# Optimization experiments

Hardware: AMD Instinct MI355X
Metric: run time of the kernel (lower is better)

Reference implementation:

```python
import jax, jax.numpy as jnp
import numpy as np
from math import ceil

N = 20000   # nodes
E = 320000  # edges
D = 128     # num_features == num_hidden
K = ceil(N * 0.1)  # 2000 PMA seeds


def _gcn(x, W, b, src, dst):
    # PyG GCNConv: add self-loops, symmetric deg^-1/2 normalization, sum-aggregate, bias
    n = x.shape[0]
    sl = jnp.arange(n)
    s = jnp.concatenate([src, sl])
    d = jnp.concatenate([dst, sl])
    deg = jax.ops.segment_sum(jnp.ones((s.shape[0],), x.dtype), d, num_segments=n)
    dinv = jax.lax.rsqrt(jnp.maximum(deg, 1e-12))
    norm = dinv[s] * dinv[d]
    h = x @ W
    return jax.ops.segment_sum(h[s] * norm[:, None], d, num_segments=n) + b


def _ln(x, g, b):
    m = jnp.mean(x, -1, keepdims=True)
    v = jnp.var(x, -1, keepdims=True)
    return (x - m) * jax.lax.rsqrt(v + 1e-5) * g + b


def setup_inputs() -> dict:
    key = jax.random.key(0)
    ks = jax.random.split(key, 32)
    w = lambda i, shape: jax.random.normal(ks[i], shape, jnp.float32) * 0.05
    z = lambda shape: jnp.zeros(shape, jnp.float32)
    o = lambda shape: jnp.ones(shape, jnp.float32)
    return {
        "x": jax.random.normal(ks[0], (N, D), jnp.float32),
        "edge_index": jax.random.randint(ks[1], (2, E), 0, N),
        "batch": jnp.zeros((N,), jnp.int32),
        "W1": w(2, (D, D)), "b1": z((D,)),
        "W2": w(3, (D, D)), "b2": z((D,)),
        "S": w(4, (1, K, D)),
        "Wq": w(5, (D, D)), "bq": z((D,)),
        "Wk": w(6, (D, D)), "bk": z((D,)),
        "Wv": w(7, (D, D)), "bv": z((D,)),
        "Wo": w(8, (D, D)), "bo": z((D,)),
        "g0": o((D,)), "be0": z((D,)),
        "g1": o((D,)), "be1": z((D,)),
        "Wl": w(9, (D, D)), "bl": z((D,)),
        "W3": w(10, (D, D)), "b3": z((D,)),
        "W4": w(11, (D, D)), "b4": z((D,)),
        "W5": w(12, (D, D)), "b5": z((D,)),
    }


def reference(x, edge_index, batch, W1, b1, W2, b2, S, Wq, bq, Wk, bk, Wv, bv,
              Wo, bo, g0, be0, g1, be1, Wl, bl, W3, b3, W4, b4, W5, b5):
    src, dst = edge_index[0], edge_index[1]
    h = jax.nn.relu(_gcn(x, W1, b1, src, dst))
    h = jax.nn.relu(_gcn(h, W2, b2, src, dst))
    # B=1 dense batch: mask all-true -> additive attention mask is 0
    Q = S @ Wq + bq                        # [1,K,D]
    Kd = _gcn(h, Wk, bk, src, dst)[None]   # [1,N,D]  (mab_conv='GCN')
    Vd = _gcn(h, Wv, bv, src, dst)[None]   # [1,N,D]
    score = jnp.einsum('bkd,bnd->bkn', Q, Kd) / jnp.sqrt(jnp.float32(D))
    A = jax.nn.softmax(score, axis=1)      # cluster=True: softmax over seed dim
    out = Q + jnp.einsum('bkn,bnd->bkd', A, Vd)
    out = _ln(out, g0, be0)
    out = out + jax.nn.relu(out @ Wo + bo)
    out = _ln(out, g1, be1)
    xl = out @ Wl + bl                     # [1,K,D]
    x_out = jnp.einsum('bkn,bkd->bnd', A, xl)[0]  # attn^T @ x -> [N,D], mask all-true
    h = jax.nn.relu(_gcn(x_out, W3, b3, src, dst))
    h = jax.nn.relu(_gcn(h, W4, b4, src, dst))
    return _gcn(h, W5, b5, src, dst)       # [N,D]
```

## Files before the change

kernel.cpp:

```cpp
#include <hip/hip_runtime.h>

#define NN 20000
#define EE 320000
#define KK 2000
#define KP 2048
#define SCALE 0.08838834764831845f
#define ZSPLIT 16
#define ACHUNKS 625

typedef const float* cfp;
typedef __attribute__((ext_vector_type(8))) short sh8;
typedef __attribute__((ext_vector_type(4))) float f32x4;

static __device__ __forceinline__ float4 ld4(const float* p){ return *reinterpret_cast<const float4*>(p); }
static __device__ __forceinline__ void st4(float* p, float4 v){ *reinterpret_cast<float4*>(p) = v; }

static __device__ __forceinline__ unsigned short f2bf(float f){
    unsigned int u = __float_as_uint(f);
    u = (u + 0x7FFFu + ((u >> 16) & 1u)) >> 16;
    return (unsigned short)u;
}
static __device__ __forceinline__ float bf2f(unsigned short h){
    return __uint_as_float(((unsigned int)h) << 16);
}
static __device__ __forceinline__ sh8 lds8(const unsigned short* p){ return *reinterpret_cast<const sh8*>(p); }

__global__ __launch_bounds__(256) void k_count(const int* dst, int* deg){
    int i = blockIdx.x*256 + threadIdx.x;
    if (i < EE) atomicAdd(&deg[dst[i]], 1);
}

__global__ __launch_bounds__(256) void k_dinv(const int* deg, float* dinv){
    int n = blockIdx.x*256 + threadIdx.x;
    if (n < NN) dinv[n] = rsqrtf((float)deg[n] + 1.0f);
}

__global__ __launch_bounds__(1024) void k_scan(const int* cnt, int* rows){
    __shared__ int part[1024];
    int t = threadIdx.x;
    int base = t*20;
    int s = 0;
    for (int i = 0; i < 20; ++i){ int idx = base+i; if (idx < NN) s += cnt[idx]; }
    part[t] = s; __syncthreads();
    for (int off = 1; off < 1024; off <<= 1){
        int v = (t >= off) ? part[t-off] : 0;
        __syncthreads();
        part[t] += v;
        __syncthreads();
    }
    int run = part[t] - s;
    for (int i = 0; i < 20; ++i){
        int idx = base+i;
        if (idx < NN){ rows[idx] = run; run += cnt[idx]; }
    }
    if (t == 0) rows[NN] = EE;
}

__global__ __launch_bounds__(256) void k_fill(const int* src, const int* dst, const int* rows,
                                              int* cursor, int* col){
    int i = blockIdx.x*256 + threadIdx.x;
    if (i < EE){
        int d = dst[i];
        int pos = rows[d] + atomicAdd(&cursor[d], 1);
        col[pos] = src[i];
    }
}

__global__ __launch_bounds__(256) void conv_wT(cfp w0, cfp w1, cfp w2, cfp w3, cfp w4, cfp w5, cfp w6,
                                               unsigned short* wts){
    const float* in;
    switch (blockIdx.z){
        case 0: in = w0; break; case 1: in = w1; break; case 2: in = w2; break;
        case 3: in = w3; break; case 4: in = w4; break; case 5: in = w5; break;
        default: in = w6; break;
    }
    unsigned short* out = wts + (size_t)blockIdx.z*16384;
    __shared__ float t[64][65];
    int r0 = blockIdx.x*64, c0 = blockIdx.y*64;
    int tid = threadIdx.x;
    for (int i = tid; i < 64*16; i += 256){
        int r = i >> 4, c4 = (i & 15) * 4;
        float4 v = ld4(in + (size_t)(r0+r)*128 + c0 + c4);
        t[r][c4+0]=v.x; t[r][c4+1]=v.y; t[r][c4+2]=v.z; t[r][c4+3]=v.w;
    }
    __syncthreads();
    for (int i = tid; i < 64*16; i += 256){
        int c = i >> 4, r4 = (i & 15) * 4;
        ushort4 o;
        o.x = f2bf(t[r4+0][c]); o.y = f2bf(t[r4+1][c]);
        o.z = f2bf(t[r4+2][c]); o.w = f2bf(t[r4+3][c]);
        *reinterpret_cast<ushort4*>(out + (size_t)(c0+c)*128 + r0 + r4) = o;
    }
}

__global__ __launch_bounds__(512) void gemm128(const float* __restrict__ A, const float* __restrict__ Wm,
                                               float* __restrict__ C, int M,
                                               const float* bias, const float* resid, int relu){
    __shared__ __align__(16) float Ws[128*132];
    __shared__ float As[64*129];
    int tid = threadIdx.x;
    int r0 = blockIdx.x*64;
    for (int i = tid; i < 128*32; i += 512){
        int r = i >> 5, c4 = (i & 31) * 4;
        float4 v = ld4(Wm + r*128 + c4);
        st4(&Ws[r*132 + c4], v);
    }
    for (int i = tid; i < 64*32; i += 512){
        int r = i >> 5, c4 = (i & 31) * 4;
        float4 v = (r0 + r < M) ? ld4(A + (size_t)(r0+r)*128 + c4) : make_float4(0,0,0,0);
        As[r*129 + c4+0] = v.x; As[r*129 + c4+1] = v.y;
        As[r*129 + c4+2] = v.z; As[r*129 + c4+3] = v.w;
    }
    __syncthreads();
    int a = tid >> 5;
    int b = tid & 31;
    float acc[4][4] = {};
    #pragma unroll 4
    for (int d = 0; d < 128; ++d){
        float4 w = ld4(&Ws[d*132 + 4*b]);
        float wv[4] = {w.x, w.y, w.z, w.w};
        float av[4];
        #pragma unroll
        for (int i = 0; i < 4; ++i) av[i] = As[(4*a+i)*129 + d];
        #pragma unroll
        for (int i = 0; i < 4; ++i)
            #pragma unroll
            for (int j = 0; j < 4; ++j)
                acc[i][j] += av[i]*wv[j];
    }
    int cc = 4*b;
    #pragma unroll
    for (int i = 0; i < 4; ++i){
        int r = r0 + 4*a + i;
        if (r < M){
            float v[4];
            #pragma unroll
            for (int j = 0; j < 4; ++j) v[j] = acc[i][j];
            if (bias){
                #pragma unroll
                for (int j = 0; j < 4; ++j) v[j] += bias[cc+j];
            }
            if (relu){
                #pragma unroll
                for (int j = 0; j < 4; ++j) v[j] = fmaxf(v[j], 0.f);
            }
            if (resid){
                float4 rv = ld4(resid + (size_t)r*128 + cc);
                v[0]+=rv.x; v[1]+=rv.y; v[2]+=rv.z; v[3]+=rv.w;
            }
            st4(C + (size_t)r*128 + cc, make_float4(v[0],v[1],v[2],v[3]));
        }
    }
}

__global__ __launch_bounds__(256) void tgemm(const unsigned short* __restrict__ A, int M,
                                             const unsigned short* __restrict__ Wt,
                                             const float* __restrict__ rscale,
                                             unsigned short* __restrict__ C){
    int tid = threadIdx.x;
    int wave = tid >> 6, lane = tid & 63;
    int wm = wave >> 1, wn = wave & 1;
    int m_base = blockIdx.x*64 + wm*32;
    int n_base = blockIdx.y*64 + wn*32;
    int l15 = lane & 15;
    int roff = (lane >> 4) * 8;
    const unsigned short* ap0 = A + (size_t)(m_base + l15)*128 + roff;
    const unsigned short* ap1 = ap0 + 16*128;
    const unsigned short* b0p = Wt + (size_t)(n_base + l15)*128 + roff;
    const unsigned short* b1p = b0p + 16*128;
    f32x4 acc00 = (f32x4)0.f, acc01 = (f32x4)0.f, acc10 = (f32x4)0.f, acc11 = (f32x4)0.f;
    #pragma unroll
    for (int r = 0; r < 128; r += 32){
        sh8 a0 = lds8(ap0 + r);
        sh8 a1 = lds8(ap1 + r);
        sh8 b0 = lds8(b0p + r);
        sh8 b1 = lds8(b1p + r);
        acc00 = __builtin_amdgcn_mfma_f32_16x16x32_bf16(a0, b0, acc00, 0, 0, 0);
        acc01 = __builtin_amdgcn_mfma_f32_16x16x32_bf16(a0, b1, acc01, 0, 0, 0);
        acc10 = __builtin_amdgcn_mfma_f32_16x16x32_bf16(a1, b0, acc10, 0, 0, 0);
        acc11 = __builtin_amdgcn_mfma_f32_16x16x32_bf16(a1, b1, acc11, 0, 0, 0);
    }
    int rq = (lane >> 4) * 4;
    f32x4 accs[2][2] = {{acc00, acc01},{acc10, acc11}};
    #pragma unroll
    for (int mi = 0; mi < 2; ++mi){
        #pragma unroll
        for (int ni = 0; ni < 2; ++ni){
            f32x4 a = accs[mi][ni];
            int gn = n_base + ni*16 + l15;
            #pragma unroll
            for (int reg = 0; reg < 4; ++reg){
                int gm = m_base + mi*16 + rq + reg;
                if (gm < M) C[(size_t)gm*128 + gn] = f2bf(a[reg] * (rscale ? rscale[gm] : 1.f));
            }
        }
    }
}

__global__ __launch_bounds__(256) void gcn_agg_bf(const unsigned short* __restrict__ y, const float* __restrict__ dinv,
                                                  const int* __restrict__ rows, const int* __restrict__ col,
                                                  const float* __restrict__ bias, void* __restrict__ outv,
                                                  int relu, int out_fp32){
    int wid = (int)((blockIdx.x*256 + threadIdx.x) >> 6);
    int lane = threadIdx.x & 63;
    if (wid >= NN) return;
    int f = lane*2;
    ushort2 u = *reinterpret_cast<const ushort2*>(y + (size_t)wid*128 + f);
    float ax = bf2f(u.x), ay = bf2f(u.y);
    int s = rows[wid], e = rows[wid+1];
    int j = s;
    int e8 = s + ((e - s) & ~7);
    for (; j < e8; j += 8){
        ushort2 v[8];
        #pragma unroll
        for (int q = 0; q < 8; ++q){
            int c = col[j+q];
            v[q] = *reinterpret_cast<const ushort2*>(y + (size_t)c*128 + f);
        }
        #pragma unroll
        for (int q = 0; q < 8; ++q){ ax += bf2f(v[q].x); ay += bf2f(v[q].y); }
    }
    for (; j < e; ++j){
        int c0 = col[j];
        ushort2 v0 = *reinterpret_cast<const ushort2*>(y + (size_t)c0*128 + f);
        ax += bf2f(v0.x); ay += bf2f(v0.y);
    }
    float dn = dinv[wid];
    float ox = ax*dn + bias[f];
    float oy = ay*dn + bias[f+1];
    if (relu){ ox = fmaxf(ox, 0.f); oy = fmaxf(oy, 0.f); }
    if (out_fp32){
        *reinterpret_cast<float2*>((float*)outv + (size_t)wid*128 + f) = make_float2(ox, oy);
    } else {
        ushort2 o; o.x = f2bf(ox); o.y = f2bf(oy);
        *reinterpret_cast<ushort2*>((unsigned short*)outv + (size_t)wid*128 + f) = o;
    }
}

__global__ __launch_bounds__(256) void conv_bf16(const float* __restrict__ in, unsigned short* __restrict__ out, int n4){
    int i = blockIdx.x*256 + threadIdx.x;
    if (i < n4){
        float4 v = ld4(in + (size_t)i*4);
        ushort4 o;
        o.x = f2bf(v.x); o.y = f2bf(v.y); o.z = f2bf(v.z); o.w = f2bf(v.w);
        *reinterpret_cast<ushort4*>(out + (size_t)i*4) = o;
    }
}

__global__ __launch_bounds__(256) void conv_bf16_T(const float* __restrict__ in, unsigned short* __restrict__ out,
                                                   int M, int ldout, const float* __restrict__ rscale){
    __shared__ float t[64][65];
    int r0 = blockIdx.x*64, c0 = blockIdx.y*64;
    int tid = threadIdx.x;
    for (int i = tid; i < 64*16; i += 256){
        int r = i >> 4, c4 = (i & 15) * 4;
        float4 v = (r0 + r < M) ? ld4(in + (size_t)(r0+r)*128 + c0 + c4) : make_float4(0,0,0,0);
        if (rscale && r0 + r < M){
            float sc = rscale[r0 + r];
            v.x *= sc; v.y *= sc; v.z *= sc; v.w *= sc;
        }
        t[r][c4+0]=v.x; t[r][c4+1]=v.y; t[r][c4+2]=v.z; t[r][c4+3]=v.w;
    }
    __syncthreads();
    for (int i = tid; i < 64*16; i += 256){
        int c = i >> 4, r4 = (i & 15) * 4;
        if (r0 + r4 < M){
            ushort4 o;
            o.x = f2bf(t[r4+0][c]); o.y = f2bf(t[r4+1][c]);
            o.z = f2bf(t[r4+2][c]); o.w = f2bf(t[r4+3][c]);
            *reinterpret_cast<ushort4*>(out + (size_t)(c0+c)*ldout + r0 + r4) = o;
        }
    }
}

__global__ __launch_bounds__(256) void k_rcp32(const float* __restrict__ zp, const float* __restrict__ dinv,
                                               float* __restrict__ zinv, float* __restrict__ zdinv){
    int n = blockIdx.x*256 + threadIdx.x;
    if (n < NN){
        float s = 0.f;
        #pragma unroll
        for (int y = 0; y < 32; ++y) s += zp[(size_t)y*NN + n];
        float zi = 1.f / s;
        zinv[n] = zi;
        zdinv[n] = zi * dinv[n];
    }
}

__global__ __launch_bounds__(256) void s_gemm_exp(const unsigned short* __restrict__ Kb,
                                                  const unsigned short* __restrict__ Qb2,
                                                  unsigned short* __restrict__ E, float* __restrict__ zpart){
    __shared__ unsigned short Es[64*68];
    int tid = threadIdx.x;
    int wave = tid >> 6, lane = tid & 63;
    int wm = wave >> 1, wn = wave & 1;
    int n_blk = blockIdx.x*64, k_blk = blockIdx.y*64;
    int l15 = lane & 15;
    int roff = (lane >> 4) * 8;
    const unsigned short* ap0 = Kb + (size_t)(n_blk + wm*32 + l15)*128 + roff;
    const unsigned short* ap1 = ap0 + 16*128;
    const unsigned short* bp0 = Qb2 + (size_t)(k_blk + wn*32 + l15)*128 + roff;
    const unsigned short* bp1 = bp0 + 16*128;
    f32x4 acc00 = (f32x4)0.f, acc01 = (f32x4)0.f, acc10 = (f32x4)0.f, acc11 = (f32x4)0.f;
    #pragma unroll
    for (int r = 0; r < 128; r += 32){
        sh8 a0 = lds8(ap0 + r);
        sh8 a1 = lds8(ap1 + r);
        sh8 b0 = lds8(bp0 + r);
        sh8 b1 = lds8(bp1 + r);
        acc00 = __builtin_amdgcn_mfma_f32_16x16x32_bf16(a0, b0, acc00, 0, 0, 0);
        acc01 = __builtin_amdgcn_mfma_f32_16x16x32_bf16(a0, b1, acc01, 0, 0, 0);
        acc10 = __builtin_amdgcn_mfma_f32_16x16x32_bf16(a1, b0, acc10, 0, 0, 0);
        acc11 = __builtin_amdgcn_mfma_f32_16x16x32_bf16(a1, b1, acc11, 0, 0, 0);
    }
    int rq = (lane >> 4) * 4;
    f32x4 accs[2][2] = {{acc00, acc01},{acc10, acc11}};
    #pragma unroll
    for (int mi = 0; mi < 2; ++mi){
        #pragma unroll
        for (int ni = 0; ni < 2; ++ni){
            f32x4 a = accs[mi][ni];
            int c_loc = wn*32 + ni*16 + l15;
            bool kv = (k_blk + c_loc) < KK;
            #pragma unroll
            for (int reg = 0; reg < 4; ++reg){
                int r_loc = wm*32 + mi*16 + rq + reg;
                float e = kv ? __expf(a[reg]*SCALE) : 0.f;
                Es[r_loc*68 + c_loc] = f2bf(e);
            }
        }
    }
    __syncthreads();
    if (tid < 64){
        int n = n_blk + tid;
        if (n < NN){
            float s = 0.f;
            #pragma unroll 8
            for (int j = 0; j < 64; ++j) s += bf2f(Es[tid*68 + j]);
            zpart[(size_t)blockIdx.y*NN + n] = s;
        }
    }
    for (int i = tid; i < 512; i += 256){
        int r = i >> 3, c8 = (i & 7) * 8;
        if (n_blk + r < NN){
            ushort4 lo = *reinterpret_cast<const ushort4*>(&Es[r*68 + c8]);
            ushort4 hi = *reinterpret_cast<const ushort4*>(&Es[r*68 + c8 + 4]);
            unsigned short* dst = E + (size_t)(n_blk + r)*KP + k_blk + c8;
            *reinterpret_cast<ushort4*>(dst) = lo;
            *reinterpret_cast<ushort4*>(dst + 4) = hi;
        }
    }
}

__global__ __launch_bounds__(256) void attn_gemm(const unsigned short* __restrict__ E,
                                                 const unsigned short* __restrict__ Vt,
                                                 float* __restrict__ part){
    __shared__ unsigned short As[64*36];
    int tid = threadIdx.x;
    int wave = tid >> 6, lane = tid & 63;
    int kk0 = blockIdx.x*64;
    int per = (ACHUNKS + ZSPLIT - 1) / ZSPLIT;
    int c0 = blockIdx.y*per;
    int c1 = min(ACHUNKS, c0 + per);
    int l15 = lane & 15;
    int q8 = (lane >> 4) * 8;
    int d0 = wave*32;
    int n_l = tid & 31;
    int k8 = (tid >> 5) * 8;
    f32x4 acc[4][2];
    #pragma unroll
    for (int g = 0; g < 4; ++g){ acc[g][0] = (f32x4)0.f; acc[g][1] = (f32x4)0.f; }
    const unsigned short* ebase = E + (size_t)n_l*KP + kk0 + k8;
    const unsigned short* vb0p = Vt + (size_t)(d0 + l15)*NN + q8;
    const unsigned short* vb1p = vb0p + (size_t)16*NN;
    sh8 etmp = lds8(ebase + (size_t)c0*32*KP);
    sh8 vb0 = lds8(vb0p + c0*32);
    sh8 vb1 = lds8(vb1p + c0*32);
    for (int ch = c0; ch < c1; ++ch){
        unsigned short tmp[8];
        *reinterpret_cast<sh8*>(tmp) = etmp;
        #pragma unroll
        for (int j = 0; j < 8; ++j) As[(k8 + j)*36 + n_l] = tmp[j];
        __syncthreads();
        sh8 etn = (sh8)0, vbn0 = (sh8)0, vbn1 = (sh8)0;
        if (ch + 1 < c1){
            etn  = lds8(ebase + (size_t)(ch+1)*32*KP);
            vbn0 = lds8(vb0p + (ch+1)*32);
            vbn1 = lds8(vb1p + (ch+1)*32);
        }
        #pragma unroll
        for (int g = 0; g < 4; ++g){
            const unsigned short* ap = &As[(g*16 + l15)*36 + q8];
            union { struct { ushort4 lo, hi; } u; sh8 v; } af;
            af.u.lo = *reinterpret_cast<const ushort4*>(ap);
            af.u.hi = *reinterpret_cast<const ushort4*>(ap + 4);
            acc[g][0] = __builtin_amdgcn_mfma_f32_16x16x32_bf16(af.v, vb0, acc[g][0], 0, 0, 0);
            acc[g][1] = __builtin_amdgcn_mfma_f32_16x16x32_bf16(af.v, vb1, acc[g][1], 0, 0, 0);
        }
        __syncthreads();
        etmp = etn; vb0 = vbn0; vb1 = vbn1;
    }
    float* pbase = part + (size_t)blockIdx.y*KK*128;
    int rq = (lane >> 4) * 4;
    #pragma unroll
    for (int g = 0; g < 4; ++g){
        #pragma unroll
        for (int ni = 0; ni < 2; ++ni){
            int d = d0 + ni*16 + l15;
            #pragma unroll
            for (int reg = 0; reg < 4; ++reg){
                int kk = kk0 + g*16 + rq + reg;
                if (kk < KK) pbase[(size_t)kk*128 + d] = acc[g][ni][reg];
            }
        }
    }
}

__global__ __launch_bounds__(256) void xout_gemm(const unsigned short* __restrict__ E,
                                                 const unsigned short* __restrict__ B,
                                                 float* __restrict__ xpart){
    int tid = threadIdx.x;
    int wave = tid >> 6, lane = tid & 63;
    int wm = wave >> 1, wn = wave & 1;
    int m_base = blockIdx.x*64 + wm*32;
    int n_base = blockIdx.y*64 + wn*32;
    int kz = blockIdx.z*1024;
    int l15 = lane & 15;
    int roff = (lane >> 4) * 8;
    const unsigned short* ap0 = E + (size_t)(m_base + l15)*KP + kz + roff;
    const unsigned short* ap1 = ap0 + (size_t)16*KP;
    const unsigned short* bp0 = B + (size_t)(n_base + l15)*KP + kz + roff;
    const unsigned short* bp1 = bp0 + (size_t)16*KP;
    f32x4 acc00 = (f32x4)0.f, acc01 = (f32x4)0.f, acc10 = (f32x4)0.f, acc11 = (f32x4)0.f;
    sh8 a0 = lds8(ap0),      a1 = lds8(ap1),      a2 = lds8(ap0 + 32), a3 = lds8(ap1 + 32);
    sh8 b0 = lds8(bp0),      b1 = lds8(bp1),      b2 = lds8(bp0 + 32), b3 = lds8(bp1 + 32);
    for (int r = 0; r < 1024; r += 64){
        int rn = r + 64;
        sh8 na0 = (sh8)0, na1 = (sh8)0, na2 = (sh8)0, na3 = (sh8)0;
        sh8 nb0 = (sh8)0, nb1 = (sh8)0, nb2 = (sh8)0, nb3 = (sh8)0;
        if (rn < 1024){
            na0 = lds8(ap0 + rn);      na1 = lds8(ap1 + rn);
            na2 = lds8(ap0 + rn + 32); na3 = lds8(ap1 + rn + 32);
            nb0 = lds8(bp0 + rn);      nb1 = lds8(bp1 + rn);
            nb2 = lds8(bp0 + rn + 32); nb3 = lds8(bp1 + rn + 32);
        }
        acc00 = __builtin_amdgcn_mfma_f32_16x16x32_bf16(a0, b0, acc00, 0, 0, 0);
        acc01 = __builtin_amdgcn_mfma_f32_16x16x32_bf16(a0, b1, acc01, 0, 0, 0);
        acc10 = __builtin_amdgcn_mfma_f32_16x16x32_bf16(a1, b0, acc10, 0, 0, 0);
        acc11 = __builtin_amdgcn_mfma_f32_16x16x32_bf16(a1, b1, acc11, 0, 0, 0);
        acc00 = __builtin_amdgcn_mfma_f32_16x16x32_bf16(a2, b2, acc00, 0, 0, 0);
        acc01 = __builtin_amdgcn_mfma_f32_16x16x32_bf16(a2, b3, acc01, 0, 0, 0);
        acc10 = __builtin_amdgcn_mfma_f32_16x16x32_bf16(a3, b2, acc10, 0, 0, 0);
        acc11 = __builtin_amdgcn_mfma_f32_16x16x32_bf16(a3, b3, acc11, 0, 0, 0);
        a0 = na0; a1 = na1; a2 = na2; a3 = na3;
        b0 = nb0; b1 = nb1; b2 = nb2; b3 = nb3;
    }
    float* pbase = xpart + (size_t)blockIdx.z*NN*128;
    int rq = (lane >> 4) * 4;
    f32x4 accs[2][2] = {{acc00, acc01},{acc10, acc11}};
    #pragma unroll
    for (int mi = 0; mi < 2; ++mi){
        #pragma unroll
        for (int ni = 0; ni < 2; ++ni){
            f32x4 a = accs[mi][ni];
            int gn = n_base + ni*16 + l15;
            #pragma unroll
            for (int reg = 0; reg < 4; ++reg){
                int gm = m_base + mi*16 + rq + reg;
                if (gm < NN) pbase[(size_t)gm*128 + gn] = a[reg];
            }
        }
    }
}

__global__ __launch_bounds__(256) void xred(const float* __restrict__ xp, const float* __restrict__ zdinv,
                                            unsigned short* __restrict__ out){
    int i = blockIdx.x*256 + threadIdx.x;
    if (i < NN*32){
        int row = i >> 5;
        float4 p0 = ld4(xp + (size_t)i*4);
        float4 p1 = ld4(xp + (size_t)NN*128 + (size_t)i*4);
        float sc = zdinv[row];
        ushort4 o;
        o.x = f2bf((p0.x + p1.x)*sc);
        o.y = f2bf((p0.y + p1.y)*sc);
        o.z = f2bf((p0.z + p1.z)*sc);
        o.w = f2bf((p0.w + p1.w)*sc);
        *reinterpret_cast<ushort4*>(out + (size_t)i*4) = o;
    }
}

__global__ __launch_bounds__(128) void ln_ker(const float* __restrict__ in, int nparts,
                                              const float* __restrict__ resid,
                                              const float* __restrict__ g, const float* __restrict__ be,
                                              float* __restrict__ out){
    __shared__ float rs[128], rq[128];
    int r = blockIdx.x, t = threadIdx.x;
    float v = 0.f;
    for (int p = 0; p < nparts; ++p) v += in[(size_t)p*KK*128 + r*128 + t];
    if (resid) v += resid[r*128 + t];
    rs[t] = v; rq[t] = v*v;
    __syncthreads();
    for (int off = 64; off > 0; off >>= 1){
        if (t < off){ rs[t] += rs[t+off]; rq[t] += rq[t+off]; }
        __syncthreads();
    }
    float mean = rs[0]*(1.f/128.f);
    float var = rq[0]*(1.f/128.f) - mean*mean;
    out[r*128 + t] = (v - mean)*rsqrtf(var + 1e-5f)*g[t] + be[t];
}

extern "C" void kernel_launch(void* const* d_in, const int* in_sizes, int n_in,
                              void* d_out, int out_size, void* d_ws, size_t ws_size,
                              hipStream_t stream){
    cfp x  = (cfp)d_in[0];
    const int* ei = (const int*)d_in[1];
    const int* esrc = ei;
    const int* edst = ei + EE;
    cfp W1=(cfp)d_in[3], b1=(cfp)d_in[4], W2=(cfp)d_in[5], b2=(cfp)d_in[6];
    cfp S =(cfp)d_in[7];
    cfp Wq=(cfp)d_in[8],  bq=(cfp)d_in[9],  Wk=(cfp)d_in[10], bk=(cfp)d_in[11];
    cfp Wv=(cfp)d_in[12], bv=(cfp)d_in[13], Wo=(cfp)d_in[14], bo=(cfp)d_in[15];
    cfp g0=(cfp)d_in[16], be0=(cfp)d_in[17], g1=(cfp)d_in[18], be1=(cfp)d_in[19];
    cfp Wl=(cfp)d_in[20], bl=(cfp)d_in[21], W3=(cfp)d_in[22], b3=(cfp)d_in[23];
    cfp W4=(cfp)d_in[24], b4=(cfp)d_in[25], W5=(cfp)d_in[26], b5=(cfp)d_in[27];

    char* wsb = (char*)d_ws;
    const size_t MB = 1048576;
    int*   deg    = (int*)  (wsb + 0);
    float* dinv   = (float*)(wsb + 81920);
    int*   rows   = (int*)  (wsb + 163840);
    int*   cursor = (int*)  (wsb + 245760);
    int*   col    = (int*)  (wsb + 327680);
    float* Qb     = (float*)(wsb + 2*MB);
    float* o1     = (float*)(wsb + 3*MB);
    float* o2     = (float*)(wsb + 4*MB);
    float* o3     = (float*)(wsb + 5*MB);
    float* xlb    = (float*)(wsb + 6*MB);
    float* zpart  = (float*)(wsb + 7*MB);
    float* zinv   = (float*)(wsb + 10*MB);
    float* zdinv  = (float*)(wsb + 10*MB + 131072);
    unsigned short* Wts  = (unsigned short*)(wsb + 10*MB + 262144);
    unsigned short* Qbf  = (unsigned short*)(wsb + 11*MB);
    unsigned short* xlt3 = (unsigned short*)(wsb + 11*MB + 524288);
    unsigned short* xbf = (unsigned short*)(wsb + 12*MB);
    unsigned short* h1  = (unsigned short*)(wsb + 17*MB);
    unsigned short* h2  = (unsigned short*)(wsb + 22*MB);
    unsigned short* ybuf= (unsigned short*)(wsb + 27*MB);
    unsigned short* Kbf = (unsigned short*)(wsb + 32*MB);
    unsigned short* Vtz = (unsigned short*)(wsb + 37*MB);
    float* NB3    = (float*)(wsb + 42*MB);
    float* part   = (float*)(wsb + 42*MB);
    float* xpart  = (float*)(wsb + 42*MB);
    unsigned short* E = (unsigned short*)(wsb + 62*MB);
    float* outp   = (float*)d_out;
    unsigned short* h3 = xbf;
    unsigned short* h4 = h1;

    (void)hipMemsetAsync(deg, 0, NN*sizeof(int), stream);
    (void)hipMemsetAsync(cursor, 0, NN*sizeof(int), stream);
    (void)hipMemsetAsync(xlt3, 0, 128*KP*sizeof(unsigned short), stream);

    k_count<<<1250, 256, 0, stream>>>(edst, deg);
    k_dinv<<<79, 256, 0, stream>>>(deg, dinv);
    k_scan<<<1, 1024, 0, stream>>>(deg, rows);
    k_fill<<<1250, 256, 0, stream>>>(esrc, edst, rows, cursor, col);

    conv_wT<<<dim3(2,2,7), 256, 0, stream>>>(W1, W2, Wk, Wv, W3, W4, W5, Wts);
    conv_bf16<<<2500, 256, 0, stream>>>(x, xbf, NN*32);
    unsigned short* W1t = Wts;
    unsigned short* W2t = Wts + 16384;
    unsigned short* Wkt = Wts + 2*16384;
    unsigned short* Wvt = Wts + 3*16384;
    unsigned short* W4t = Wts + 5*16384;
    unsigned short* W5t = Wts + 6*16384;

    const int GN = 313;
    const int GK = 32;

    tgemm<<<dim3(GN,2), 256, 0, stream>>>(xbf, NN, W1t, dinv, ybuf);
    gcn_agg_bf<<<5000, 256, 0, stream>>>(ybuf, dinv, rows, col, b1, h1, 1, 0);
    tgemm<<<dim3(GN,2), 256, 0, stream>>>(h1, NN, W2t, dinv, ybuf);
    gcn_agg_bf<<<5000, 256, 0, stream>>>(ybuf, dinv, rows, col, b2, h2, 1, 0);
    tgemm<<<dim3(GN,2), 256, 0, stream>>>(h2, NN, Wkt, dinv, ybuf);
    gcn_agg_bf<<<5000, 256, 0, stream>>>(ybuf, dinv, rows, col, bk, Kbf, 0, 0);
    gemm128<<<GK, 512, 0, stream>>>(S, Wq, Qb, KK, bq, nullptr, 0);
    conv_bf16<<<250, 256, 0, stream>>>(Qb, Qbf, KK*32);
    s_gemm_exp<<<dim3(GN, GK), 256, 0, stream>>>(Kbf, Qbf, E, zpart);
    k_rcp32<<<79, 256, 0, stream>>>(zpart, dinv, zinv, zdinv);
    tgemm<<<dim3(GN,2), 256, 0, stream>>>(h2, NN, Wvt, dinv, ybuf);
    gcn_agg_bf<<<5000, 256, 0, stream>>>(ybuf, dinv, rows, col, bv, NB3, 0, 1);
    conv_bf16_T<<<dim3(GN, 2), 256, 0, stream>>>(NB3, Vtz, NN, NN, zinv);
    attn_gemm<<<dim3(GK, ZSPLIT), 256, 0, stream>>>(E, Vtz, part);
    ln_ker<<<KK, 128, 0, stream>>>(part, ZSPLIT, Qb, g0, be0, o1);
    gemm128<<<GK, 512, 0, stream>>>(o1, Wo, o2, KK, bo, o1, 1);
    ln_ker<<<KK, 128, 0, stream>>>(o2, 1, nullptr, g1, be1, o3);
    gemm128<<<GK, 512, 0, stream>>>(o3, Wl, xlb, KK, bl, nullptr, 0);
    gemm128<<<GK, 512, 0, stream>>>(xlb, W3, o1, KK, nullptr, nullptr, 0);
    conv_bf16_T<<<dim3(GK, 2), 256, 0, stream>>>(o1, xlt3, KK, KP, nullptr);
    xout_gemm<<<dim3(GN, 2, 2), 256, 0, stream>>>(E, xlt3, xpart);
    xred<<<2500, 256, 0, stream>>>(xpart, zdinv, ybuf);
    gcn_agg_bf<<<5000, 256, 0, stream>>>(ybuf, dinv, rows, col, b3, h3, 1, 0);
    tgemm<<<dim3(GN,2), 256, 0, stream>>>(h3, NN, W4t, dinv, ybuf);
    gcn_agg_bf<<<5000, 256, 0, stream>>>(ybuf, dinv, rows, col, b4, h4, 1, 0);
    tgemm<<<dim3(GN,2), 256, 0, stream>>>(h4, NN, W5t, dinv, ybuf);
    gcn_agg_bf<<<5000, 256, 0, stream>>>(ybuf, dinv, rows, col, b5, outp, 0, 1);
}
```

Baseline: 632.7 us.

## Fuse dinv into scan, bf16 Q output, retile GEMMs, nontemporal E loads/stores

Several independent changes. The dinv computation moves into the scan kernel, and the Q GEMM writes a bf16 copy directly, which drops the separate conversion kernel. The node-feature GEMM is retiled so each block covers 32 rows by the full 128 columns in one grid dimension, and the score GEMM handles 128 seeds per block, halving its grid and the z-partial count. The large E matrix is written and read with nontemporal hints to reduce cache pollution. The trade-offs are different occupancy and register pressure from the larger per-wave tiles.

```diff
diff --git a/kernel.cpp b/kernel.cpp
--- a/kernel.cpp
+++ b/kernel.cpp
@@ -24,18 +24,16 @@
     return __uint_as_float(((unsigned int)h) << 16);
 }
 static __device__ __forceinline__ sh8 lds8(const unsigned short* p){ return *reinterpret_cast<const sh8*>(p); }
+static __device__ __forceinline__ sh8 ldnt8(const unsigned short* p){
+    return __builtin_nontemporal_load(reinterpret_cast<const sh8*>(p));
+}
 
 __global__ __launch_bounds__(256) void k_count(const int* dst, int* deg){
     int i = blockIdx.x*256 + threadIdx.x;
     if (i < EE) atomicAdd(&deg[dst[i]], 1);
 }
 
-__global__ __launch_bounds__(256) void k_dinv(const int* deg, float* dinv){
-    int n = blockIdx.x*256 + threadIdx.x;
-    if (n < NN) dinv[n] = rsqrtf((float)deg[n] + 1.0f);
-}
-
-__global__ __launch_bounds__(1024) void k_scan(const int* cnt, int* rows){
+__global__ __launch_bounds__(1024) void k_scan(const int* cnt, int* rows, float* dinv){
     __shared__ int part[1024];
     int t = threadIdx.x;
     int base = t*20;
@@ -51,7 +49,10 @@
     int run = part[t] - s;
     for (int i = 0; i < 20; ++i){
         int idx = base+i;
-        if (idx < NN){ rows[idx] = run; run += cnt[idx]; }
+        if (idx < NN){
+            rows[idx] = run; run += cnt[idx];
+            dinv[idx] = rsqrtf((float)cnt[idx] + 1.0f);
+        }
     }
     if (t == 0) rows[NN] = EE;
 }
@@ -95,7 +96,8 @@
 
 __global__ __launch_bounds__(512) void gemm128(const float* __restrict__ A, const float* __restrict__ Wm,
                                                float* __restrict__ C, int M,
-                                               const float* bias, const float* resid, int relu){
+                                               const float* bias, const float* resid, int relu,
+                                               unsigned short* __restrict__ Cbf){
     __shared__ __align__(16) float Ws[128*132];
     __shared__ float As[64*129];
     int tid = threadIdx.x;
@@ -149,6 +151,11 @@
                 v[0]+=rv.x; v[1]+=rv.y; v[2]+=rv.z; v[3]+=rv.w;
             }
             st4(C + (size_t)r*128 + cc, make_float4(v[0],v[1],v[2],v[3]));
+            if (Cbf){
+                ushort4 o;
+                o.x = f2bf(v[0]); o.y = f2bf(v[1]); o.z = f2bf(v[2]); o.w = f2bf(v[3]);
+                *reinterpret_cast<ushort4*>(Cbf + (size_t)r*128 + cc) = o;
+            }
         }
     }
 }
@@ -160,39 +167,31 @@
     int tid = threadIdx.x;
     int wave = tid >> 6, lane = tid & 63;
     int wm = wave >> 1, wn = wave & 1;
-    int m_base = blockIdx.x*64 + wm*32;
-    int n_base = blockIdx.y*64 + wn*32;
+    int m_base = blockIdx.x*32 + wm*16;
     int l15 = lane & 15;
     int roff = (lane >> 4) * 8;
-    const unsigned short* ap0 = A + (size_t)(m_base + l15)*128 + roff;
-    const unsigned short* ap1 = ap0 + 16*128;
-    const unsigned short* b0p = Wt + (size_t)(n_base + l15)*128 + roff;
-    const unsigned short* b1p = b0p + 16*128;
-    f32x4 acc00 = (f32x4)0.f, acc01 = (f32x4)0.f, acc10 = (f32x4)0.f, acc11 = (f32x4)0.f;
+    const unsigned short* ap = A + (size_t)(m_base + l15)*128 + roff;
+    const unsigned short* bp = Wt + (size_t)(wn*64 + l15)*128 + roff;
+    f32x4 acc[4];
+    #pragma unroll
+    for (int j = 0; j < 4; ++j) acc[j] = (f32x4)0.f;
     #pragma unroll
     for (int r = 0; r < 128; r += 32){
-        sh8 a0 = lds8(ap0 + r);
-        sh8 a1 = lds8(ap1 + r);
-        sh8 b0 = lds8(b0p + r);
-        sh8 b1 = lds8(b1p + r);
-        acc00 = __builtin_amdgcn_mfma_f32_16x16x32_bf16(a0, b0, acc00, 0, 0, 0);
-        acc01 = __builtin_amdgcn_mfma_f32_16x16x32_bf16(a0, b1, acc01, 0, 0, 0);
-        acc10 = __builtin_amdgcn_mfma_f32_16x16x32_bf16(a1, b0, acc10, 0, 0, 0);
-        acc11 = __builtin_amdgcn_mfma_f32_16x16x32_bf16(a1, b1, acc11, 0, 0, 0);
+        sh8 a = lds8(ap + r);
+        #pragma unroll
+        for (int j = 0; j < 4; ++j){
+            sh8 b = lds8(bp + j*16*128 + r);
+            acc[j] = __builtin_amdgcn_mfma_f32_16x16x32_bf16(a, b, acc[j], 0, 0, 0);
+        }
     }
     int rq = (lane >> 4) * 4;
-    f32x4 accs[2][2] = {{acc00, acc01},{acc10, acc11}};
-    #pragma unroll
-    for (int mi = 0; mi < 2; ++mi){
-        #pragma unroll
-        for (int ni = 0; ni < 2; ++ni){
-            f32x4 a = accs[mi][ni];
-            int gn = n_base + ni*16 + l15;
-            #pragma unroll
-            for (int reg = 0; reg < 4; ++reg){
-                int gm = m_base + mi*16 + rq + reg;
-                if (gm < M) C[(size_t)gm*128 + gn] = f2bf(a[reg] * (rscale ? rscale[gm] : 1.f));
-            }
+    #pragma unroll
+    for (int ni = 0; ni < 4; ++ni){
+        int gn = wn*64 + ni*16 + l15;
+        #pragma unroll
+        for (int reg = 0; reg < 4; ++reg){
+            int gm = m_base + rq + reg;
+            if (gm < M) C[(size_t)gm*128 + gn] = f2bf(acc[ni][reg] * (rscale ? rscale[gm] : 1.f));
         }
     }
 }
@@ -279,7 +278,7 @@
     if (n < NN){
         float s = 0.f;
         #pragma unroll
-        for (int y = 0; y < 32; ++y) s += zp[(size_t)y*NN + n];
+        for (int y = 0; y < 16; ++y) s += zp[(size_t)y*NN + n];
         float zi = 1.f / s;
         zinv[n] = zi;
         zdinv[n] = zi * dinv[n];
@@ -289,43 +288,45 @@
 __global__ __launch_bounds__(256) void s_gemm_exp(const unsigned short* __restrict__ Kb,
                                                   const unsigned short* __restrict__ Qb2,
                                                   unsigned short* __restrict__ E, float* __restrict__ zpart){
-    __shared__ unsigned short Es[64*68];
+    __shared__ unsigned short Es[64*136];
     int tid = threadIdx.x;
     int wave = tid >> 6, lane = tid & 63;
     int wm = wave >> 1, wn = wave & 1;
-    int n_blk = blockIdx.x*64, k_blk = blockIdx.y*64;
+    int n_blk = blockIdx.x*64, k_blk = blockIdx.y*128;
     int l15 = lane & 15;
     int roff = (lane >> 4) * 8;
     const unsigned short* ap0 = Kb + (size_t)(n_blk + wm*32 + l15)*128 + roff;
     const unsigned short* ap1 = ap0 + 16*128;
-    const unsigned short* bp0 = Qb2 + (size_t)(k_blk + wn*32 + l15)*128 + roff;
-    const unsigned short* bp1 = bp0 + 16*128;
-    f32x4 acc00 = (f32x4)0.f, acc01 = (f32x4)0.f, acc10 = (f32x4)0.f, acc11 = (f32x4)0.f;
+    const unsigned short* bp = Qb2 + (size_t)(k_blk + wn*64 + l15)*128 + roff;
+    f32x4 acc[2][4];
+    #pragma unroll
+    for (int mi = 0; mi < 2; ++mi)
+        #pragma unroll
+        for (int j = 0; j < 4; ++j) acc[mi][j] = (f32x4)0.f;
     #pragma unroll
     for (int r = 0; r < 128; r += 32){
         sh8 a0 = lds8(ap0 + r);
         sh8 a1 = lds8(ap1 + r);
-        sh8 b0 = lds8(bp0 + r);
-        sh8 b1 = lds8(bp1 + r);
-        acc00 = __builtin_amdgcn_mfma_f32_16x16x32_bf16(a0, b0, acc00, 0, 0, 0);
-        acc01 = __builtin_amdgcn_mfma_f32_16x16x32_bf16(a0, b1, acc01, 0, 0, 0);
-        acc10 = __builtin_amdgcn_mfma_f32_16x16x32_bf16(a1, b0, acc10, 0, 0, 0);
-        acc11 = __builtin_amdgcn_mfma_f32_16x16x32_bf16(a1, b1, acc11, 0, 0, 0);
+        #pragma unroll
+        for (int j = 0; j < 4; ++j){
+            sh8 b = lds8(bp + j*16*128 + r);
+            acc[0][j] = __builtin_amdgcn_mfma_f32_16x16x32_bf16(a0, b, acc[0][j], 0, 0, 0);
+            acc[1][j] = __builtin_amdgcn_mfma_f32_16x16x32_bf16(a1, b, acc[1][j], 0, 0, 0);
+        }
     }
     int rq = (lane >> 4) * 4;
-    f32x4 accs[2][2] = {{acc00, acc01},{acc10, acc11}};
     #pragma unroll
     for (int mi = 0; mi < 2; ++mi){
         #pragma unroll
-        for (int ni = 0; ni < 2; ++ni){
-            f32x4 a = accs[mi][ni];
-            int c_loc = wn*32 + ni*16 + l15;
+        for (int ni = 0; ni < 4; ++ni){
+            f32x4 a = acc[mi][ni];
+            int c_loc = wn*64 + ni*16 + l15;
             bool kv = (k_blk + c_loc) < KK;
             #pragma unroll
             for (int reg = 0; reg < 4; ++reg){
                 int r_loc = wm*32 + mi*16 + rq + reg;
                 float e = kv ? __expf(a[reg]*SCALE) : 0.f;
-                Es[r_loc*68 + c_loc] = f2bf(e);
+                Es[r_loc*136 + c_loc] = f2bf(e);
             }
         }
     }
@@ -335,18 +336,19 @@
         if (n < NN){
             float s = 0.f;
             #pragma unroll 8
-            for (int j = 0; j < 64; ++j) s += bf2f(Es[tid*68 + j]);
+            for (int j = 0; j < 128; ++j) s += bf2f(Es[tid*136 + j]);
             zpart[(size_t)blockIdx.y*NN + n] = s;
         }
     }
-    for (int i = tid; i < 512; i += 256){
-        int r = i >> 3, c8 = (i & 7) * 8;
+    for (int i = tid; i < 1024; i += 256){
+        int r = i >> 4, c8 = (i & 15) * 8;
         if (n_blk + r < NN){
-            ushort4 lo = *reinterpret_cast<const ushort4*>(&Es[r*68 + c8]);
-            ushort4 hi = *reinterpret_cast<const ushort4*>(&Es[r*68 + c8 + 4]);
-            unsigned short* dst = E + (size_t)(n_blk + r)*KP + k_blk + c8;
-            *reinterpret_cast<ushort4*>(dst) = lo;
-            *reinterpret_cast<ushort4*>(dst + 4) = hi;
+            sh8 v = lds8(&Es[r*136 + c8]);
+            union { sh8 s; unsigned long long q[2]; } u;
+            u.s = v;
+            unsigned long long* dst = reinterpret_cast<unsigned long long*>(E + (size_t)(n_blk + r)*KP + k_blk + c8);
+            __builtin_nontemporal_store(u.q[0], dst);
+            __builtin_nontemporal_store(u.q[1], dst + 1);
         }
     }
 }
@@ -372,7 +374,7 @@
     const unsigned short* ebase = E + (size_t)n_l*KP + kk0 + k8;
     const unsigned short* vb0p = Vt + (size_t)(d0 + l15)*NN + q8;
     const unsigned short* vb1p = vb0p + (size_t)16*NN;
-    sh8 etmp = lds8(ebase + (size_t)c0*32*KP);
+    sh8 etmp = ldnt8(ebase + (size_t)c0*32*KP);
     sh8 vb0 = lds8(vb0p + c0*32);
     sh8 vb1 = lds8(vb1p + c0*32);
     for (int ch = c0; ch < c1; ++ch){
@@ -383,7 +385,7 @@
         __syncthreads();
         sh8 etn = (sh8)0, vbn0 = (sh8)0, vbn1 = (sh8)0;
         if (ch + 1 < c1){
-            etn  = lds8(ebase + (size_t)(ch+1)*32*KP);
+            etn  = ldnt8(ebase + (size_t)(ch+1)*32*KP);
             vbn0 = lds8(vb0p + (ch+1)*32);
             vbn1 = lds8(vb1p + (ch+1)*32);
         }
@@ -431,17 +433,17 @@
     const unsigned short* bp0 = B + (size_t)(n_base + l15)*KP + kz + roff;
     const unsigned short* bp1 = bp0 + (size_t)16*KP;
     f32x4 acc00 = (f32x4)0.f, acc01 = (f32x4)0.f, acc10 = (f32x4)0.f, acc11 = (f32x4)0.f;
-    sh8 a0 = lds8(ap0),      a1 = lds8(ap1),      a2 = lds8(ap0 + 32), a3 = lds8(ap1 + 32);
-    sh8 b0 = lds8(bp0),      b1 = lds8(bp1),      b2 = lds8(bp0 + 32), b3 = lds8(bp1 + 32);
+    sh8 a0 = ldnt8(ap0),      a1 = ldnt8(ap1),      a2 = ldnt8(ap0 + 32), a3 = ldnt8(ap1 + 32);
+    sh8 b0 = lds8(bp0),       b1 = lds8(bp1),       b2 = lds8(bp0 + 32),  b3 = lds8(bp1 + 32);
     for (int r = 0; r < 1024; r += 64){
         int rn = r + 64;
         sh8 na0 = (sh8)0, na1 = (sh8)0, na2 = (sh8)0, na3 = (sh8)0;
         sh8 nb0 = (sh8)0, nb1 = (sh8)0, nb2 = (sh8)0, nb3 = (sh8)0;
         if (rn < 1024){
-            na0 = lds8(ap0 + rn);      na1 = lds8(ap1 + rn);
-            na2 = lds8(ap0 + rn + 32); na3 = lds8(ap1 + rn + 32);
-            nb0 = lds8(bp0 + rn);      nb1 = lds8(bp1 + rn);
-            nb2 = lds8(bp0 + rn + 32); nb3 = lds8(bp1 + rn + 32);
+            na0 = ldnt8(ap0 + rn);      na1 = ldnt8(ap1 + rn);
+            na2 = ldnt8(ap0 + rn + 32); na3 = ldnt8(ap1 + rn + 32);
+            nb0 = lds8(bp0 + rn);       nb1 = lds8(bp1 + rn);
+            nb2 = lds8(bp0 + rn + 32);  nb3 = lds8(bp1 + rn + 32);
         }
         acc00 = __builtin_amdgcn_mfma_f32_16x16x32_bf16(a0, b0, acc00, 0, 0, 0);
         acc01 = __builtin_amdgcn_mfma_f32_16x16x32_bf16(a0, b1, acc01, 0, 0, 0);
@@ -561,8 +563,7 @@
     (void)hipMemsetAsync(xlt3, 0, 128*KP*sizeof(unsigned short), stream);
 
     k_count<<<1250, 256, 0, stream>>>(edst, deg);
-    k_dinv<<<79, 256, 0, stream>>>(deg, dinv);
-    k_scan<<<1, 1024, 0, stream>>>(deg, rows);
+    k_scan<<<1, 1024, 0, stream>>>(deg, rows, dinv);
     k_fill<<<1250, 256, 0, stream>>>(esrc, edst, rows, cursor, col);
 
     conv_wT<<<dim3(2,2,7), 256, 0, stream>>>(W1, W2, Wk, Wv, W3, W4, W5, Wts);
@@ -575,33 +576,33 @@
     unsigned short* W5t = Wts + 6*16384;
 
     const int GN = 313;
+    const int GT = 625;
     const int GK = 32;
 
-    tgemm<<<dim3(GN,2), 256, 0, stream>>>(xbf, NN, W1t, dinv, ybuf);
+    tgemm<<<GT, 256, 0, stream>>>(xbf, NN, W1t, dinv, ybuf);
     gcn_agg_bf<<<5000, 256, 0, stream>>>(ybuf, dinv, rows, col, b1, h1, 1, 0);
-    tgemm<<<dim3(GN,2), 256, 0, stream>>>(h1, NN, W2t, dinv, ybuf);
+    tgemm<<<GT, 256, 0, stream>>>(h1, NN, W2t, dinv, ybuf);
     gcn_agg_bf<<<5000, 256, 0, stream>>>(ybuf, dinv, rows, col, b2, h2, 1, 0);
-    tgemm<<<dim3(GN,2), 256, 0, stream>>>(h2, NN, Wkt, dinv, ybuf);
+    tgemm<<<GT, 256, 0, stream>>>(h2, NN, Wkt, dinv, ybuf);
     gcn_agg_bf<<<5000, 256, 0, stream>>>(ybuf, dinv, rows, col, bk, Kbf, 0, 0);
-    gemm128<<<GK, 512, 0, stream>>>(S, Wq, Qb, KK, bq, nullptr, 0);
-    conv_bf16<<<250, 256, 0, stream>>>(Qb, Qbf, KK*32);
-    s_gemm_exp<<<dim3(GN, GK), 256, 0, stream>>>(Kbf, Qbf, E, zpart);
+    gemm128<<<GK, 512, 0, stream>>>(S, Wq, Qb, KK, bq, nullptr, 0, Qbf);
+    s_gemm_exp<<<dim3(GN, 16), 256, 0, stream>>>(Kbf, Qbf, E, zpart);
     k_rcp32<<<79, 256, 0, stream>>>(zpart, dinv, zinv, zdinv);
-    tgemm<<<dim3(GN,2), 256, 0, stream>>>(h2, NN, Wvt, dinv, ybuf);
+    tgemm<<<GT, 256, 0, stream>>>(h2, NN, Wvt, dinv, ybuf);
     gcn_agg_bf<<<5000, 256, 0, stream>>>(ybuf, dinv, rows, col, bv, NB3, 0, 1);
     conv_bf16_T<<<dim3(GN, 2), 256, 0, stream>>>(NB3, Vtz, NN, NN, zinv);
     attn_gemm<<<dim3(GK, ZSPLIT), 256, 0, stream>>>(E, Vtz, part);
     ln_ker<<<KK, 128, 0, stream>>>(part, ZSPLIT, Qb, g0, be0, o1);
-    gemm128<<<GK, 512, 0, stream>>>(o1, Wo, o2, KK, bo, o1, 1);
+    gemm128<<<GK, 512, 0, stream>>>(o1, Wo, o2, KK, bo, o1, 1, nullptr);
     ln_ker<<<KK, 128, 0, stream>>>(o2, 1, nullptr, g1, be1, o3);
-    gemm128<<<GK, 512, 0, stream>>>(o3, Wl, xlb, KK, bl, nullptr, 0);
-    gemm128<<<GK, 512, 0, stream>>>(xlb, W3, o1, KK, nullptr, nullptr, 0);
+    gemm128<<<GK, 512, 0, stream>>>(o3, Wl, xlb, KK, bl, nullptr, 0, nullptr);
+    gemm128<<<GK, 512, 0, stream>>>(xlb, W3, o1, KK, nullptr, nullptr, 0, nullptr);
     conv_bf16_T<<<dim3(GK, 2), 256, 0, stream>>>(o1, xlt3, KK, KP, nullptr);
     xout_gemm<<<dim3(GN, 2, 2), 256, 0, stream>>>(E, xlt3, xpart);
     xred<<<2500, 256, 0, stream>>>(xpart, zdinv, ybuf);
     gcn_agg_bf<<<5000, 256, 0, stream>>>(ybuf, dinv, rows, col, b3, h3, 1, 0);
-    tgemm<<<dim3(GN,2), 256, 0, stream>>>(h3, NN, W4t, dinv, ybuf);
+    tgemm<<<GT, 256, 0, stream>>>(h3, NN, W4t, dinv, ybuf);
     gcn_agg_bf<<<5000, 256, 0, stream>>>(ybuf, dinv, rows, col, b4, h4, 1, 0);
-    tgemm<<<dim3(GN,2), 256, 0, stream>>>(h4, NN, W5t, dinv, ybuf);
+    tgemm<<<GT, 256, 0, stream>>>(h4, NN, W5t, dinv, ybuf);
     gcn_agg_bf<<<5000, 256, 0, stream>>>(ybuf, dinv, rows, col, b5, outp, 0, 1);
 }
```

After: 691.1 us. +9.2%, slower.
